# Optimization experiments

Measured on AMD Instinct MI355X. Metric: run time of the kernel, lower is better.

## Reference

```python
import jax, jax.numpy as jnp
import numpy as np

B, NX, NY = 4, 128, 128
DIM, DH, HEADS, LATENT, DOUT = 128, 64, 8, 64, 128
KM = 3
KD = DH * KM          # per-head low-rank-kernel dim (192)
SCALING = 1.0         # kernel_multiplier<=4 and softmax=False -> scaling_factor
ROT_SCALE = 64.0      # 1/min_freq of continuous RotaryEmbedding (min_freq=1/64)
EPS = 1e-5


def layer_norm(x, g, b):
    m = x.mean(-1, keepdims=True)
    v = jnp.var(x, axis=-1, keepdims=True)
    return (x - m) * jax.lax.rsqrt(v + EPS) * g + b


def pooling_reducer(x, Win, g, b, W1, b1, W2, b2):
    # x: [b, n, m, c] -> mean over axis 2 -> PreNorm(MLP with gated GELU) -> [b, n, latent]
    h = (x @ Win).mean(axis=2)
    h = layer_norm(h, g, b)
    h = h @ W1 + b1
    c = h.shape[-1] // 2
    h = jax.nn.gelu(h[..., :c], approximate=False) * h[..., c:]
    return h @ W2 + b2


def rotary(t, pos):
    # t: [b,h,n,d], pos: [n] continuous coordinates
    d = t.shape[-1]
    inv_freq = 1.0 / (10000.0 ** (jnp.arange(0, d, 2, dtype=jnp.float32) / d))
    f = (pos * ROT_SCALE)[:, None] * inv_freq          # [n, d//2]
    f = jnp.concatenate([f, f], axis=-1)               # [n, d]
    cos, sin = jnp.cos(f), jnp.sin(f)
    x1, x2 = jnp.split(t, 2, axis=-1)
    rot = jnp.concatenate([-x2, x1], axis=-1)          # rotate_half (half-split variant)
    return t * cos + rot * sin


def low_rank_kernel(u, pos, Wqk):
    # u: [b, n, latent] -> kernel K: [b, h, n, n]
    b, n, _ = u.shape
    qk = u @ Wqk                                       # [b, n, 2*h*KD]
    q, k = jnp.split(qk, 2, axis=-1)
    q = q.reshape(b, n, HEADS, KD).transpose(0, 2, 1, 3)
    k = k.reshape(b, n, HEADS, KD).transpose(0, 2, 1, 3)
    q = rotary(q, pos)
    k = rotary(k, pos)
    return jnp.einsum('bhid,bhjd->bhij', q, k) * SCALING


def setup_inputs():
    key = jax.random.key(0)
    ks = jax.random.split(key, 16)
    s = 0.02
    def rn(k, shape):
        return jax.random.normal(k, shape, dtype=jnp.float32) * s
    return {
        'u': jax.random.normal(ks[0], (B, NX, NY, DIM), dtype=jnp.float32),
        'pos_x': jnp.sort(jax.random.uniform(ks[1], (NX,), dtype=jnp.float32)),
        'pos_y': jnp.sort(jax.random.uniform(ks[2], (NY,), dtype=jnp.float32)),
        'ln_g': jnp.ones((DIM,), jnp.float32),
        'ln_b': jnp.zeros((DIM,), jnp.float32),
        'Wv': rn(ks[3], (DIM, HEADS * DH)),
        'Win': rn(ks[4], (DIM, DIM)),
        'px_Win': rn(ks[5], (DIM, DIM)),
        'px_g': jnp.ones((DIM,), jnp.float32),
        'px_b': jnp.zeros((DIM,), jnp.float32),
        'px_W1': rn(ks[6], (DIM, 2 * DIM)),
        'px_b1': jnp.zeros((2 * DIM,), jnp.float32),
        'px_W2': rn(ks[7], (DIM, LATENT)),
        'px_b2': jnp.zeros((LATENT,), jnp.float32),
        'py_Win': rn(ks[8], (DIM, DIM)),
        'py_g': jnp.ones((DIM,), jnp.float32),
        'py_b': jnp.zeros((DIM,), jnp.float32),
        'py_W1': rn(ks[9], (DIM, 2 * DIM)),
        'py_b1': jnp.zeros((2 * DIM,), jnp.float32),
        'py_W2': rn(ks[10], (DIM, LATENT)),
        'py_b2': jnp.zeros((LATENT,), jnp.float32),
        'Wqk_x': rn(ks[11], (LATENT, 2 * HEADS * KD)),
        'Wqk_y': rn(ks[12], (LATENT, 2 * HEADS * KD)),
        'Wo1': rn(ks[13], (HEADS * DH, DOUT)),
        'Wo2': rn(ks[14], (DOUT, DOUT)),
    }


def reference(u, pos_x, pos_y, ln_g, ln_b, Wv, Win,
              px_Win, px_g, px_b, px_W1, px_b1, px_W2, px_b2,
              py_Win, py_g, py_b, py_W1, py_b1, py_W2, py_b2,
              Wqk_x, Wqk_y, Wo1, Wo2):
    un = layer_norm(u, ln_g, ln_b)                      # [b,nx,ny,dim]
    v = un @ Wv                                         # [b,nx,ny,h*dh]
    ui = un @ Win
    ux = pooling_reducer(ui, px_Win, px_g, px_b, px_W1, px_b1, px_W2, px_b2)                       # [b,nx,L]
    uy = pooling_reducer(ui.transpose(0, 2, 1, 3), py_Win, py_g, py_b, py_W1, py_b1, py_W2, py_b2)  # [b,ny,L]
    kx = low_rank_kernel(ux, pos_x, Wqk_x)              # [b,h,nx,nx]
    ky = low_rank_kernel(uy, pos_y, Wqk_y)              # [b,h,ny,ny]
    b, nx, ny, _ = u.shape
    vphi = v.reshape(b, nx, ny, HEADS, DH).transpose(0, 3, 1, 2, 4)   # b h i l c
    t = jnp.einsum('bhij,bhjmc->bhimc', kx, vphi)       # attend along x axis
    t = jnp.einsum('bhlm,bhimc->bhilc', ky, t)          # attend along y axis
    t = t.transpose(0, 2, 3, 1, 4).reshape(b, nx, ny, HEADS * DH)
    # InstanceNorm2d applied to a channels-LAST tensor (as in the original repo):
    # torch treats dim1 (nx) as channels, normalizing over (ny, h*dh) per (b, nx), no affine.
    m = t.mean(axis=(2, 3), keepdims=True)
    var = t.var(axis=(2, 3), keepdims=True)
    t = (t - m) * jax.lax.rsqrt(var + EPS)
    h = jax.nn.gelu(t @ Wo1, approximate=False)
    return h @ Wo2
```

## Files before the change

kernel.cpp:

```cpp
#include <hip/hip_runtime.h>
#include <math.h>

#define ROWS 65536
#define KDD 192

typedef __attribute__((ext_vector_type(8))) short bfrag;
typedef __attribute__((ext_vector_type(4))) float facc;

__device__ inline unsigned short bf16r(float x) {
  union { float f; unsigned u; } v; v.f = x;
  unsigned r = v.u + 0x7fffu + ((v.u >> 16) & 1u);
  return (unsigned short)(r >> 16);
}
__device__ inline float bf2f(unsigned short h) {
  union { unsigned u; float f; } v; v.u = ((unsigned)h) << 16; return v.f;
}
__device__ inline float gelu_f(float x) {
  return x * 0.5f * (1.f + erff(x * 0.70710678f));
}

__global__ __launch_bounds__(128) void k_ln(const float* __restrict__ x,
                                            const float* __restrict__ g,
                                            const float* __restrict__ bb,
                                            unsigned short* __restrict__ y) {
  int row = blockIdx.x;
  int t = threadIdx.x;
  float v = x[(size_t)row * 128 + t];
  float s = v, s2 = v * v;
  for (int off = 32; off > 0; off >>= 1) {
    s += __shfl_down(s, off, 64);
    s2 += __shfl_down(s2, off, 64);
  }
  __shared__ float ps[2], ps2[2];
  int wid = t >> 6, lane = t & 63;
  if (lane == 0) { ps[wid] = s; ps2[wid] = s2; }
  __syncthreads();
  float S = ps[0] + ps[1], S2 = ps2[0] + ps2[1];
  float mean = S * (1.f / 128.f);
  float var = S2 * (1.f / 128.f) - mean * mean;
  float r = rsqrtf(var + 1e-5f);
  y[(size_t)row * 128 + t] = bf16r((v - mean) * r * g[t] + bb[t]);
}

__global__ __launch_bounds__(128) void k_means(const unsigned short* __restrict__ un,
                                               float* __restrict__ mx, float* __restrict__ my) {
  int blk = blockIdx.x;
  int c = threadIdx.x;
  if (blk < 512) {
    const unsigned short* p = un + (size_t)blk * 16384 + c;
    float s = 0;
    for (int j = 0; j < 128; j++) s += bf2f(p[(size_t)j * 128]);
    mx[(size_t)blk * 128 + c] = s * (1.f / 128.f);
  } else {
    int bj = blk - 512;
    int b = bj >> 7, j = bj & 127;
    const unsigned short* p = un + (size_t)b * 2097152 + (size_t)j * 128 + c;
    float s = 0;
    for (int i = 0; i < 128; i++) s += bf2f(p[(size_t)i * 16384]);
    my[(size_t)bj * 128 + c] = s * (1.f / 128.f);
  }
}

__global__ __launch_bounds__(256) void k_wprep(const float* __restrict__ Wv,
                                               const float* __restrict__ Wo1,
                                               const float* __restrict__ Wo2,
                                               unsigned short* __restrict__ WvT,
                                               unsigned short* __restrict__ Wo1T,
                                               unsigned short* __restrict__ Wo2T,
                                               float* __restrict__ scol) {
  int blk = blockIdx.x, t = threadIdx.x;
  if (blk < 256) {
    int idx = blk * 256 + t;
    int c = idx >> 7, r = idx & 127;
    WvT[(size_t)c * 128 + r] = bf16r(Wv[(size_t)r * 512 + c]);
  } else if (blk < 512) {
    int idx = (blk - 256) * 256 + t;
    int n = idx >> 9, k = idx & 511;
    Wo1T[(size_t)n * 512 + k] = bf16r(Wo1[(size_t)k * 128 + n]);
  } else if (blk < 576) {
    int idx = (blk - 512) * 256 + t;
    int n = idx >> 7, k = idx & 127;
    Wo2T[n * 128 + k] = bf16r(Wo2[k * 128 + n]);
  } else {
    if (t < 128) {
      float a = 0;
      for (int k = 0; k < 512; k++) a += bf2f(bf16r(Wo1[k * 128 + t]));
      scol[t] = a;
    }
  }
}

__global__ __launch_bounds__(256) void k_gemmz(const float* __restrict__ A0,
                                               const float* __restrict__ B0,
                                               float* __restrict__ C0,
                                               const float* __restrict__ A1,
                                               const float* __restrict__ B1,
                                               float* __restrict__ C1,
                                               int K, int lda, int ldb, int ldc) {
  const float* A = blockIdx.z ? A1 : A0;
  const float* Bm = blockIdx.z ? B1 : B0;
  float* C = blockIdx.z ? C1 : C0;
  __shared__ float As[16][64];
  __shared__ float Bs[16][64];
  int tid = threadIdx.x;
  int n0 = blockIdx.x * 64, m0 = blockIdx.y * 64;
  int tx = tid & 15, ty = tid >> 4;
  float acc[4][4] = {};
  int la_m = tid >> 2, la_k = (tid & 3) * 4;
  int lb_k = tid >> 4, lb_n = (tid & 15) * 4;
  for (int k0 = 0; k0 < K; k0 += 16) {
    float4 a4 = *(const float4*)(A + (size_t)(m0 + la_m) * lda + k0 + la_k);
    As[la_k + 0][la_m] = a4.x; As[la_k + 1][la_m] = a4.y;
    As[la_k + 2][la_m] = a4.z; As[la_k + 3][la_m] = a4.w;
    float4 b4 = *(const float4*)(Bm + (size_t)(k0 + lb_k) * ldb + n0 + lb_n);
    *(float4*)&Bs[lb_k][lb_n] = b4;
    __syncthreads();
#pragma unroll
    for (int kk = 0; kk < 16; kk++) {
      float4 av = *(const float4*)&As[kk][ty * 4];
      float4 bv = *(const float4*)&Bs[kk][tx * 4];
      float a[4] = {av.x, av.y, av.z, av.w};
      float b[4] = {bv.x, bv.y, bv.z, bv.w};
#pragma unroll
      for (int i = 0; i < 4; i++)
#pragma unroll
        for (int j = 0; j < 4; j++) acc[i][j] += a[i] * b[j];
    }
    __syncthreads();
  }
#pragma unroll
  for (int i = 0; i < 4; i++) {
    float4 o;
    o.x = acc[i][0]; o.y = acc[i][1]; o.z = acc[i][2]; o.w = acc[i][3];
    *(float4*)(C + (size_t)(m0 + ty * 4 + i) * ldc + n0 + tx * 4) = o;
  }
}

__global__ __launch_bounds__(128) void k_pool2(const float* __restrict__ in0, const float* __restrict__ in1,
                                               const float* __restrict__ Wc0, const float* __restrict__ Wc1,
                                               const float* __restrict__ g0, const float* __restrict__ g1,
                                               const float* __restrict__ bb0, const float* __restrict__ bb1,
                                               const float* __restrict__ W10, const float* __restrict__ W11,
                                               const float* __restrict__ b10, const float* __restrict__ b11,
                                               const float* __restrict__ W20, const float* __restrict__ W21,
                                               const float* __restrict__ b20, const float* __restrict__ b21,
                                               float* __restrict__ o0, float* __restrict__ o1) {
  int sel = blockIdx.y;
  const float* in = sel ? in1 : in0;  const float* Wc = sel ? Wc1 : Wc0;
  const float* g = sel ? g1 : g0;     const float* bb = sel ? bb1 : bb0;
  const float* W1 = sel ? W11 : W10;  const float* b1 = sel ? b11 : b10;
  const float* W2 = sel ? W21 : W20;  const float* b2 = sel ? b21 : b20;
  float* out = sel ? o1 : o0;
  int row = blockIdx.x;
  int t = threadIdx.x;
  __shared__ float xin[128], h1[128], h3[128];
  __shared__ float ps[2], ps2[2];
  xin[t] = in[(size_t)row * 128 + t];
  __syncthreads();
  float a = 0;
  for (int k = 0; k < 128; k++) a += xin[k] * Wc[k * 128 + t];
  float s = a, s2 = a * a;
  for (int off = 32; off > 0; off >>= 1) {
    s += __shfl_down(s, off, 64);
    s2 += __shfl_down(s2, off, 64);
  }
  if ((t & 63) == 0) { ps[t >> 6] = s; ps2[t >> 6] = s2; }
  __syncthreads();
  float S = ps[0] + ps[1], S2 = ps2[0] + ps2[1];
  float mean = S * (1.f / 128.f);
  float var = S2 * (1.f / 128.f) - mean * mean;
  float r = rsqrtf(var + 1e-5f);
  h1[t] = (a - mean) * r * g[t] + bb[t];
  __syncthreads();
  float u1 = b1[t], u2 = b1[t + 128];
  for (int k = 0; k < 128; k++) {
    float hv = h1[k];
    u1 += hv * W1[k * 256 + t];
    u2 += hv * W1[k * 256 + t + 128];
  }
  h3[t] = gelu_f(u1) * u2;
  __syncthreads();
  if (t < 64) {
    float o = b2[t];
    for (int k = 0; k < 128; k++) o += h3[k] * W2[k * 64 + t];
    out[(size_t)row * 64 + t] = o;
  }
}

__global__ __launch_bounds__(192) void k_rot2(const float* __restrict__ qk0, const float* __restrict__ qk1,
                                              const float* __restrict__ pos0, const float* __restrict__ pos1,
                                              float* __restrict__ qr0, float* __restrict__ qr1,
                                              float* __restrict__ kr0, float* __restrict__ kr1) {
  int sel = blockIdx.y;
  const float* qk = sel ? qk1 : qk0;
  const float* pos = sel ? pos1 : pos0;
  float* qr = sel ? qr1 : qr0;
  float* kr = sel ? kr1 : kr0;
  int bn = blockIdx.x;
  int b = bn >> 7, n = bn & 127;
  int d = threadIdx.x;
  int fi = d % 96;
  float inv = expf(-logf(10000.f) * ((float)fi / 96.f));
  float f = pos[n] * 64.f * inv;
  float cs = cosf(f), sn = sinf(f);
  int partner = d < 96 ? d + 96 : d - 96;
  float sgn = d < 96 ? -1.f : 1.f;
  for (int h = 0; h < 8; h++) {
    float q = qk[(size_t)bn * 3072 + h * 192 + d];
    float qp = qk[(size_t)bn * 3072 + h * 192 + partner];
    float kx = qk[(size_t)bn * 3072 + 1536 + h * 192 + d];
    float kp = qk[(size_t)bn * 3072 + 1536 + h * 192 + partner];
    size_t o = ((size_t)(b * 8 + h) * 128 + n) * 192 + d;
    qr[o] = q * cs + sgn * qp * sn;
    kr[o] = kx * cs + sgn * kp * sn;
  }
}

__global__ __launch_bounds__(256) void k_qkt2(const float* __restrict__ Q0, const float* __restrict__ K0,
                                              unsigned short* __restrict__ C0,
                                              const float* __restrict__ Q1, const float* __restrict__ K1,
                                              unsigned short* __restrict__ C1) {
  int z = blockIdx.z;
  int bh = z & 31;
  const float* Qb = (z < 32 ? Q0 : Q1) + (size_t)bh * 128 * KDD;
  const float* Kb = (z < 32 ? K0 : K1) + (size_t)bh * 128 * KDD;
  unsigned short* Cb = (z < 32 ? C0 : C1) + (size_t)bh * 128 * 128;
  __shared__ float As[16][64];
  __shared__ float Bs[16][64];
  int tid = threadIdx.x;
  int i0 = blockIdx.y * 64, j0 = blockIdx.x * 64;
  int tx = tid & 15, ty = tid >> 4;
  float acc[4][4] = {};
  int l_m = tid >> 2, l_k = (tid & 3) * 4;
  for (int k0 = 0; k0 < KDD; k0 += 16) {
    float4 a4 = *(const float4*)(Qb + (size_t)(i0 + l_m) * KDD + k0 + l_k);
    As[l_k + 0][l_m] = a4.x; As[l_k + 1][l_m] = a4.y;
    As[l_k + 2][l_m] = a4.z; As[l_k + 3][l_m] = a4.w;
    float4 b4 = *(const float4*)(Kb + (size_t)(j0 + l_m) * KDD + k0 + l_k);
    Bs[l_k + 0][l_m] = b4.x; Bs[l_k + 1][l_m] = b4.y;
    Bs[l_k + 2][l_m] = b4.z; Bs[l_k + 3][l_m] = b4.w;
    __syncthreads();
#pragma unroll
    for (int kk = 0; kk < 16; kk++) {
      float4 av = *(const float4*)&As[kk][ty * 4];
      float4 bv = *(const float4*)&Bs[kk][tx * 4];
      float a[4] = {av.x, av.y, av.z, av.w};
      float b[4] = {bv.x, bv.y, bv.z, bv.w};
#pragma unroll
      for (int i = 0; i < 4; i++)
#pragma unroll
        for (int j = 0; j < 4; j++) acc[i][j] += a[i] * b[j];
    }
    __syncthreads();
  }
#pragma unroll
  for (int i = 0; i < 4; i++) {
    unsigned h0 = bf16r(acc[i][0]), h1 = bf16r(acc[i][1]);
    unsigned h2 = bf16r(acc[i][2]), h3 = bf16r(acc[i][3]);
    uint2 pk;
    pk.x = h0 | (h1 << 16);
    pk.y = h2 | (h3 << 16);
    *(uint2*)(Cb + (size_t)(i0 + ty * 4 + i) * 128 + j0 + tx * 4) = pk;
  }
}


__global__ __launch_bounds__(256) void k_vt(const unsigned short* __restrict__ WvT,
                                            const unsigned short* __restrict__ un,
                                            unsigned short* __restrict__ vT) {
  int nt = blockIdx.x;
  int mt = blockIdx.y;
  __shared__ __align__(16) unsigned short As[16384];
  __shared__ __align__(16) unsigned short Bs[16384];
  int tid = threadIdx.x;
  int w = tid >> 6, lane = tid & 63, quad = lane >> 4, l16 = lane & 15;
  {
    int r = tid >> 1, half = tid & 1;
    const unsigned short* sa = WvT + (size_t)(mt * 128 + r) * 128 + half * 64;
    const unsigned short* sbp = un + (size_t)(nt * 128 + r) * 128 + half * 64;
#pragma unroll
    for (int q = 0; q < 8; q++) {
      int c8 = half * 8 + q;
      int ph = ((c8 ^ (r & 15)) << 3);
      *(uint4*)&As[r * 128 + ph] = *(const uint4*)(sa + q * 8);
      *(uint4*)&Bs[r * 128 + ph] = *(const uint4*)(sbp + q * 8);
    }
  }
  __syncthreads();
  facc zf = {0.f, 0.f, 0.f, 0.f};
  facc acc[2][8];
#pragma unroll
  for (int a = 0; a < 2; a++)
#pragma unroll
    for (int bq = 0; bq < 8; bq++) acc[a][bq] = zf;
#pragma unroll
  for (int k0 = 0; k0 < 4; k0++) {
    bfrag av[2];
#pragma unroll
    for (int it = 0; it < 2; it++) {
      int row = (w + it * 4) * 16 + l16;
      av[it] = *(const bfrag*)&As[row * 128 + ((((k0 * 4 + quad) ^ l16)) << 3)];
    }
#pragma unroll
    for (int nt8 = 0; nt8 < 8; nt8++) {
      int row = nt8 * 16 + l16;
      bfrag bv = *(const bfrag*)&Bs[row * 128 + ((((k0 * 4 + quad) ^ l16)) << 3)];
      acc[0][nt8] = __builtin_amdgcn_mfma_f32_16x16x32_bf16(av[0], bv, acc[0][nt8], 0, 0, 0);
      acc[1][nt8] = __builtin_amdgcn_mfma_f32_16x16x32_bf16(av[1], bv, acc[1][nt8], 0, 0, 0);
    }
  }
  __syncthreads();
#pragma unroll
  for (int it = 0; it < 2; it++)
#pragma unroll
    for (int nt8 = 0; nt8 < 8; nt8++)
#pragma unroll
      for (int rr = 0; rr < 4; rr++) {
        int row = (w + it * 4) * 16 + quad * 4 + rr;
        int col = nt8 * 16 + l16;
        As[row * 128 + ((((col >> 3) ^ (row & 15)) << 3)) + (col & 7)] = bf16r(acc[it][nt8][rr]);
      }
  __syncthreads();
  {
    int r = tid >> 1, half = tid & 1;
    unsigned short* dst = vT + (size_t)(mt * 128 + r) * 65536 + (size_t)nt * 128 + half * 64;
#pragma unroll
    for (int q = 0; q < 8; q++) {
      int c8 = half * 8 + q;
      *(uint4*)(dst + q * 8) = *(const uint4*)&As[r * 128 + ((c8 ^ (r & 15)) << 3)];
    }
  }
}

__global__ __launch_bounds__(256) void k_fuse12(const unsigned short* __restrict__ kxall,
                                                const unsigned short* __restrict__ kyall,
                                                const unsigned short* __restrict__ vT,
                                                unsigned short* __restrict__ ttp,
                                                float* __restrict__ sb,
                                                float* __restrict__ s2b) {
  int blk = blockIdx.x;
  int bh = blk >> 4, strip = blk & 15;
  int b = bh >> 3, h = bh & 7;
  __shared__ __align__(16) unsigned short Ky[16384];
  __shared__ __align__(16) unsigned short Vs[16384];
  __shared__ float sL[128], s2L[128];
  int tid = threadIdx.x;
  int w = tid >> 6, lane = tid & 63, quad = lane >> 4, l16 = lane & 15;
  if (tid < 128) { sL[tid] = 0.f; s2L[tid] = 0.f; }
  {
    int r = tid >> 1, half = tid & 1;
    const unsigned short* s = kyall + (size_t)bh * 16384 + (size_t)r * 128 + half * 64;
#pragma unroll
    for (int q = 0; q < 8; q++) {
      int c8 = half * 8 + q;
      *(uint4*)&Ky[r * 128 + ((c8 ^ (r & 15)) << 3)] = *(const uint4*)(s + q * 8);
    }
  }
  uint4 axf[2][4];
#pragma unroll
  for (int it = 0; it < 2; it++) {
    int i = (w + it * 4) * 16 + l16;
#pragma unroll
    for (int k0 = 0; k0 < 4; k0++)
      axf[it][k0] = *(const uint4*)(kxall + (size_t)bh * 16384 + (size_t)i * 128 + k0 * 32 + quad * 8);
  }
  __syncthreads();
  facc zf = {0.f, 0.f, 0.f, 0.f};
  for (int cc = 0; cc < 4; cc++) {
    int c = strip * 4 + cc;
    if (cc) __syncthreads();
    {
      int r = tid >> 1, half = tid & 1;
      const unsigned short* s = vT + (size_t)(h * 64 + c) * 65536 + (size_t)b * 16384 +
                                (size_t)r * 128 + half * 64;
#pragma unroll
      for (int q = 0; q < 8; q++) {
        int c8 = half * 8 + q;
        *(uint4*)&Vs[r * 128 + ((c8 ^ (r & 15)) << 3)] = *(const uint4*)(s + q * 8);
      }
    }
    __syncthreads();
    facc a1[2][8];
#pragma unroll
    for (int a = 0; a < 2; a++)
#pragma unroll
      for (int bq = 0; bq < 8; bq++) a1[a][bq] = zf;
#pragma unroll
    for (int k0 = 0; k0 < 4; k0++) {
      bfrag av[2];
#pragma unroll
      for (int it = 0; it < 2; it++) {
        int row = (w + it * 4) * 16 + l16;
        av[it] = *(const bfrag*)&Vs[row * 128 + (((k0 * 4 + quad) ^ l16) << 3)];
      }
#pragma unroll
      for (int lt = 0; lt < 8; lt++) {
        int row = lt * 16 + l16;
        bfrag bv = *(const bfrag*)&Ky[row * 128 + (((k0 * 4 + quad) ^ l16) << 3)];
        a1[0][lt] = __builtin_amdgcn_mfma_f32_16x16x32_bf16(av[0], bv, a1[0][lt], 0, 0, 0);
        a1[1][lt] = __builtin_amdgcn_mfma_f32_16x16x32_bf16(av[1], bv, a1[1][lt], 0, 0, 0);
      }
    }
    __syncthreads();
#pragma unroll
    for (int it = 0; it < 2; it++)
#pragma unroll
      for (int lt = 0; lt < 8; lt++)
#pragma unroll
        for (int rr = 0; rr < 4; rr++) {
          int j = (w + it * 4) * 16 + quad * 4 + rr;
          int l = lt * 16 + l16;
          Vs[l * 128 + (((j >> 3) ^ (l & 15)) << 3) + (j & 7)] = bf16r(a1[it][lt][rr]);
        }
    __syncthreads();
    facc a2[2][8];
#pragma unroll
    for (int a = 0; a < 2; a++)
#pragma unroll
      for (int bq = 0; bq < 8; bq++) a2[a][bq] = zf;
#pragma unroll
    for (int k0 = 0; k0 < 4; k0++) {
      bfrag av0 = *(const bfrag*)&axf[0][k0];
      bfrag av1 = *(const bfrag*)&axf[1][k0];
#pragma unroll
      for (int lt = 0; lt < 8; lt++) {
        int row = lt * 16 + l16;
        bfrag bv = *(const bfrag*)&Vs[row * 128 + (((k0 * 4 + quad) ^ l16) << 3)];
        a2[0][lt] = __builtin_amdgcn_mfma_f32_16x16x32_bf16(av0, bv, a2[0][lt], 0, 0, 0);
        a2[1][lt] = __builtin_amdgcn_mfma_f32_16x16x32_bf16(av1, bv, a2[1][lt], 0, 0, 0);
      }
    }
    __syncthreads();
#pragma unroll
    for (int it = 0; it < 2; it++)
#pragma unroll
      for (int lt = 0; lt < 8; lt++)
#pragma unroll
        for (int rr = 0; rr < 4; rr++) {
          int i = (w + it * 4) * 16 + quad * 4 + rr;
          int l = lt * 16 + l16;
          Vs[i * 128 + (((l >> 3) ^ (i & 15)) << 3) + (l & 7)] = bf16r(a2[it][lt][rr]);
        }
    __syncthreads();
    {
      int r = tid >> 1, half = tid & 1;
      float s = 0.f, s2 = 0.f;
      unsigned short* dst = ttp + ((size_t)(bh * 64 + c) * 128 + r) * 128 + half * 64;
#pragma unroll
      for (int q = 0; q < 8; q++) {
        int c8 = half * 8 + q;
        uint4 v = *(const uint4*)&Vs[r * 128 + ((c8 ^ (r & 15)) << 3)];
        *(uint4*)(dst + q * 8) = v;
        unsigned short* pv = (unsigned short*)&v;
#pragma unroll
        for (int e = 0; e < 8; e++) { float f = bf2f(pv[e]); s += f; s2 += f * f; }
      }
      atomicAdd(&sL[r], s);
      atomicAdd(&s2L[r], s2);
    }
  }
  __syncthreads();
  if (tid < 128) {
    atomicAdd(&sb[b * 128 + tid], sL[tid]);
    atomicAdd(&s2b[b * 128 + tid], s2L[tid]);
  }
}

__global__ __launch_bounds__(256) void k_tail2(const unsigned short* __restrict__ ttp,
                                               const unsigned short* __restrict__ Wo1T,
                                               const unsigned short* __restrict__ Wo2T,
                                               float* __restrict__ out,
                                               const float* __restrict__ sb,
                                               const float* __restrict__ s2b,
                                               const float* __restrict__ sc) {
  int blk = blockIdx.x;
  int b = blk >> 7, i = blk & 127;
  __shared__ __align__(16) unsigned short As[16384];
  __shared__ __align__(16) unsigned short Bs[16384];
  int tid = threadIdx.x;
  int w = tid >> 6, lane = tid & 63, quad = lane >> 4, l16 = lane & 15;
  facc zf = {0.f, 0.f, 0.f, 0.f};
  facc a1[2][8];
#pragma unroll
  for (int a = 0; a < 2; a++)
#pragma unroll
    for (int bq = 0; bq < 8; bq++) a1[a][bq] = zf;
  for (int kc = 0; kc < 4; kc++) {
    if (kc) __syncthreads();
    {
      int r = tid >> 1, half = tid & 1;
      int hc = kc * 128 + r;
      const unsigned short* src = ttp + (((size_t)(b * 8 + (hc >> 6)) * 64 + (hc & 63)) * 128 + i) * 128 + half * 64;
#pragma unroll
      for (int q = 0; q < 8; q++) {
        uint4 v = *(const uint4*)(src + q * 8);
        unsigned short* pv = (unsigned short*)&v;
#pragma unroll
        for (int e = 0; e < 8; e++) {
          int l = half * 64 + q * 8 + e;
          As[l * 128 + (((r >> 3) ^ (l & 15)) << 3) + (r & 7)] = pv[e];
        }
      }
      const unsigned short* sB = Wo1T + (size_t)r * 512 + kc * 128 + half * 64;
#pragma unroll
      for (int q = 0; q < 8; q++) {
        int c8 = half * 8 + q;
        *(uint4*)&Bs[r * 128 + ((c8 ^ (r & 15)) << 3)] = *(const uint4*)(sB + q * 8);
      }
    }
    __syncthreads();
#pragma unroll
    for (int k0 = 0; k0 < 4; k0++) {
      bfrag av[2];
#pragma unroll
      for (int it = 0; it < 2; it++) {
        int row = (w + it * 4) * 16 + l16;
        av[it] = *(const bfrag*)&As[row * 128 + (((k0 * 4 + quad) ^ l16) << 3)];
      }
#pragma unroll
      for (int nt = 0; nt < 8; nt++) {
        int row = nt * 16 + l16;
        bfrag bv = *(const bfrag*)&Bs[row * 128 + (((k0 * 4 + quad) ^ l16) << 3)];
        a1[0][nt] = __builtin_amdgcn_mfma_f32_16x16x32_bf16(av[0], bv, a1[0][nt], 0, 0, 0);
        a1[1][nt] = __builtin_amdgcn_mfma_f32_16x16x32_bf16(av[1], bv, a1[1][nt], 0, 0, 0);
      }
    }
  }
  float S = sb[b * 128 + i], S2 = s2b[b * 128 + i];
  float mean = S * (1.f / 65536.f);
  float var = S2 * (1.f / 65536.f) - mean * mean;
  float rs = rsqrtf(var + 1e-5f);
  __syncthreads();
#pragma unroll
  for (int it = 0; it < 2; it++)
#pragma unroll
    for (int nt = 0; nt < 8; nt++) {
      int n1 = nt * 16 + l16;
      float scn = sc[n1];
#pragma unroll
      for (int rr = 0; rr < 4; rr++) {
        int l = (w + it * 4) * 16 + quad * 4 + rr;
        float val = (a1[it][nt][rr] - mean * scn) * rs;
        As[l * 128 + (((n1 >> 3) ^ (l & 15)) << 3) + (n1 & 7)] = bf16r(gelu_f(val));
      }
    }
  {
    int r = tid >> 1, half = tid & 1;
    const unsigned short* sB = Wo2T + (size_t)r * 128 + half * 64;
#pragma unroll
    for (int q = 0; q < 8; q++) {
      int c8 = half * 8 + q;
      *(uint4*)&Bs[r * 128 + ((c8 ^ (r & 15)) << 3)] = *(const uint4*)(sB + q * 8);
    }
  }
  __syncthreads();
  facc a2[2][8];
#pragma unroll
  for (int a = 0; a < 2; a++)
#pragma unroll
    for (int bq = 0; bq < 8; bq++) a2[a][bq] = zf;
#pragma unroll
  for (int k0 = 0; k0 < 4; k0++) {
    bfrag av[2];
#pragma unroll
    for (int it = 0; it < 2; it++) {
      int row = (w + it * 4) * 16 + l16;
      av[it] = *(const bfrag*)&As[row * 128 + (((k0 * 4 + quad) ^ l16) << 3)];
    }
#pragma unroll
    for (int nt = 0; nt < 8; nt++) {
      int row = nt * 16 + l16;
      bfrag bv = *(const bfrag*)&Bs[row * 128 + (((k0 * 4 + quad) ^ l16) << 3)];
      a2[0][nt] = __builtin_amdgcn_mfma_f32_16x16x32_bf16(av[0], bv, a2[0][nt], 0, 0, 0);
      a2[1][nt] = __builtin_amdgcn_mfma_f32_16x16x32_bf16(av[1], bv, a2[1][nt], 0, 0, 0);
    }
  }
#pragma unroll
  for (int it = 0; it < 2; it++)
#pragma unroll
    for (int nt = 0; nt < 8; nt++) {
      int n2 = nt * 16 + l16;
#pragma unroll
      for (int rr = 0; rr < 4; rr++) {
        int l = (w + it * 4) * 16 + quad * 4 + rr;
        out[((size_t)(b * 16384 + i * 128 + l)) * 128 + n2] = a2[it][nt][rr];
      }
    }
}

extern "C" void kernel_launch(void* const* d_in, const int* in_sizes, int n_in,
                              void* d_out, int out_size, void* d_ws, size_t ws_size,
                              hipStream_t stream) {
  const float* u = (const float*)d_in[0];
  const float* pos_x = (const float*)d_in[1];
  const float* pos_y = (const float*)d_in[2];
  const float* ln_g = (const float*)d_in[3];
  const float* ln_b = (const float*)d_in[4];
  const float* Wv = (const float*)d_in[5];
  const float* Win = (const float*)d_in[6];
  const float* px_Win = (const float*)d_in[7];
  const float* px_g = (const float*)d_in[8];
  const float* px_b = (const float*)d_in[9];
  const float* px_W1 = (const float*)d_in[10];
  const float* px_b1 = (const float*)d_in[11];
  const float* px_W2 = (const float*)d_in[12];
  const float* px_b2 = (const float*)d_in[13];
  const float* py_Win = (const float*)d_in[14];
  const float* py_g = (const float*)d_in[15];
  const float* py_b = (const float*)d_in[16];
  const float* py_W1 = (const float*)d_in[17];
  const float* py_b1 = (const float*)d_in[18];
  const float* py_W2 = (const float*)d_in[19];
  const float* py_b2 = (const float*)d_in[20];
  const float* Wqk_x = (const float*)d_in[21];
  const float* Wqk_y = (const float*)d_in[22];
  const float* Wo1 = (const float*)d_in[23];
  const float* Wo2 = (const float*)d_in[24];
  float* out = (float*)d_out;

  const size_t NEED = 44868736;
  if (ws_size < NEED * sizeof(float)) return;
  float* ws = (float*)d_ws;
  unsigned short* un_bf = (unsigned short*)ws;
  unsigned short* vT    = (unsigned short*)(ws + 4194304);
  unsigned short* ttp   = (unsigned short*)(ws + 20971520);
  float* small = ws + 37748736;
  float* mun_x = small;
  float* mun_y = small + 65536;
  float* Wcx   = small + 131072;
  float* Wcy   = small + 147456;
  float* ux    = small + 163840;
  float* uy    = small + 196608;
  float* qkx   = small + 229376;
  float* qky   = small + 1802240;
  float* qrx   = small + 3375104;
  float* krx   = small + 4161536;
  float* qry   = small + 4947968;
  float* kry   = small + 5734400;
  unsigned short* kx_bf = (unsigned short*)(small + 6520832);
  unsigned short* ky_bf = (unsigned short*)(small + 6782976);
  unsigned short* WvT   = (unsigned short*)(small + 7045120);
  unsigned short* Wo1T  = (unsigned short*)(small + 7077888);
  unsigned short* Wo2T  = (unsigned short*)(small + 7110656);
  float* sbuf  = small + 7118848;
  float* s2buf = small + 7119360;
  float* scol  = small + 7119872;

  hipMemsetAsync(sbuf, 0, 1024 * sizeof(float), stream);

  k_ln<<<ROWS, 128, 0, stream>>>(u, ln_g, ln_b, un_bf);
  k_means<<<1024, 128, 0, stream>>>(un_bf, mun_x, mun_y);
  k_wprep<<<577, 256, 0, stream>>>(Wv, Wo1, Wo2, WvT, Wo1T, Wo2T, scol);
  k_gemmz<<<dim3(2, 2, 2), 256, 0, stream>>>(Win, px_Win, Wcx, Win, py_Win, Wcy,
                                             128, 128, 128, 128);
  k_pool2<<<dim3(512, 2), 128, 0, stream>>>(mun_x, mun_y, Wcx, Wcy, px_g, py_g, px_b, py_b,
                                            px_W1, py_W1, px_b1, py_b1, px_W2, py_W2,
                                            px_b2, py_b2, ux, uy);
  k_gemmz<<<dim3(48, 8, 2), 256, 0, stream>>>(ux, Wqk_x, qkx, uy, Wqk_y, qky,
                                              64, 64, 3072, 3072);
  k_rot2<<<dim3(512, 2), 192, 0, stream>>>(qkx, qky, pos_x, pos_y, qrx, qry, krx, kry);
  k_qkt2<<<dim3(2, 2, 64), 256, 0, stream>>>(qrx, krx, kx_bf, qry, kry, ky_bf);

  k_vt<<<dim3(512, 4), 256, 0, stream>>>(WvT, un_bf, vT);
  k_fuse12<<<512, 256, 0, stream>>>(kx_bf, ky_bf, vT, ttp, sbuf, s2buf);
  k_tail2<<<512, 256, 0, stream>>>(ttp, Wo1T, Wo2T, out, sbuf, s2buf, scol);
}
```

Before: 350.1 us.

## Restructure fused axial-attention kernel with 2x2 warp tiling and direct-to-LDS loads

After: 337.2 us. -3.7%, faster.

```diff
diff --git a/kernel.cpp b/kernel.cpp
--- a/kernel.cpp
+++ b/kernel.cpp
@@ -17,6 +17,11 @@
 }
 __device__ inline float gelu_f(float x) {
   return x * 0.5f * (1.f + erff(x * 0.70710678f));
+}
+__device__ __forceinline__ void gload16(const void* g, void* l) {
+  __builtin_amdgcn_global_load_lds((const __attribute__((address_space(1))) unsigned int*)g,
+                                   (__attribute__((address_space(3))) unsigned int*)l,
+                                   16, 0, 0);
 }
 
 __global__ __launch_bounds__(128) void k_ln(const float* __restrict__ x,
@@ -332,137 +337,148 @@
   }
 }
 
-__global__ __launch_bounds__(256) void k_fuse12(const unsigned short* __restrict__ kxall,
-                                                const unsigned short* __restrict__ kyall,
-                                                const unsigned short* __restrict__ vT,
-                                                unsigned short* __restrict__ ttp,
-                                                float* __restrict__ sb,
-                                                float* __restrict__ s2b) {
+__global__ __launch_bounds__(256, 2) void k_fuse12(const unsigned short* __restrict__ kxall,
+                                                   const unsigned short* __restrict__ kyall,
+                                                   const unsigned short* __restrict__ vT,
+                                                   unsigned short* __restrict__ ttp,
+                                                   float* __restrict__ sb,
+                                                   float* __restrict__ s2b) {
   int blk = blockIdx.x;
   int bh = blk >> 4, strip = blk & 15;
   int b = bh >> 3, h = bh & 7;
   __shared__ __align__(16) unsigned short Ky[16384];
   __shared__ __align__(16) unsigned short Vs[16384];
-  __shared__ float sL[128], s2L[128];
   int tid = threadIdx.x;
   int w = tid >> 6, lane = tid & 63, quad = lane >> 4, l16 = lane & 15;
-  if (tid < 128) { sL[tid] = 0.f; s2L[tid] = 0.f; }
+  int wr = w >> 1, wc = w & 1;
+
   {
-    int r = tid >> 1, half = tid & 1;
-    const unsigned short* s = kyall + (size_t)bh * 16384 + (size_t)r * 128 + half * 64;
+    const unsigned short* kb = kyall + (size_t)bh * 16384;
 #pragma unroll
     for (int q = 0; q < 8; q++) {
-      int c8 = half * 8 + q;
-      *(uint4*)&Ky[r * 128 + ((c8 ^ (r & 15)) << 3)] = *(const uint4*)(s + q * 8);
-    }
-  }
-  uint4 axf[2][4];
-#pragma unroll
-  for (int it = 0; it < 2; it++) {
-    int i = (w + it * 4) * 16 + l16;
-#pragma unroll
-    for (int k0 = 0; k0 < 4; k0++)
-      axf[it][k0] = *(const uint4*)(kxall + (size_t)bh * 16384 + (size_t)i * 128 + k0 * 32 + quad * 8);
-  }
-  __syncthreads();
+      int rbase = w * 32 + q * 4;
+      int r = rbase + quad;
+      gload16(kb + (size_t)r * 128 + ((l16 ^ (r & 15)) << 3), &Ky[rbase * 128]);
+    }
+  }
+  bfrag axf[4][4];
+  {
+    const unsigned short* xb = kxall + (size_t)bh * 16384;
+#pragma unroll
+    for (int it = 0; it < 4; it++) {
+      int i = (wr * 4 + it) * 16 + l16;
+#pragma unroll
+      for (int k0 = 0; k0 < 4; k0++)
+        axf[it][k0] = *(const bfrag*)(xb + (size_t)i * 128 + k0 * 32 + quad * 8);
+    }
+  }
+
+  float s[4] = {0.f, 0.f, 0.f, 0.f}, s2[4] = {0.f, 0.f, 0.f, 0.f};
   facc zf = {0.f, 0.f, 0.f, 0.f};
+
   for (int cc = 0; cc < 4; cc++) {
     int c = strip * 4 + cc;
     if (cc) __syncthreads();
     {
-      int r = tid >> 1, half = tid & 1;
-      const unsigned short* s = vT + (size_t)(h * 64 + c) * 65536 + (size_t)b * 16384 +
-                                (size_t)r * 128 + half * 64;
+      const unsigned short* vb = vT + (size_t)(h * 64 + c) * 65536 + (size_t)b * 16384;
 #pragma unroll
       for (int q = 0; q < 8; q++) {
-        int c8 = half * 8 + q;
-        *(uint4*)&Vs[r * 128 + ((c8 ^ (r & 15)) << 3)] = *(const uint4*)(s + q * 8);
-      }
-    }
-    __syncthreads();
-    facc a1[2][8];
-#pragma unroll
-    for (int a = 0; a < 2; a++)
-#pragma unroll
-      for (int bq = 0; bq < 8; bq++) a1[a][bq] = zf;
+        int rbase = w * 32 + q * 4;
+        int r = rbase + quad;
+        gload16(vb + (size_t)r * 128 + ((l16 ^ (r & 15)) << 3), &Vs[rbase * 128]);
+      }
+    }
+    __syncthreads();
+
+    facc a1[4][4];
+#pragma unroll
+    for (int xt = 0; xt < 4; xt++)
+#pragma unroll
+      for (int lt = 0; lt < 4; lt++) a1[xt][lt] = zf;
 #pragma unroll
     for (int k0 = 0; k0 < 4; k0++) {
-      bfrag av[2];
-#pragma unroll
-      for (int it = 0; it < 2; it++) {
-        int row = (w + it * 4) * 16 + l16;
-        av[it] = *(const bfrag*)&Vs[row * 128 + (((k0 * 4 + quad) ^ l16) << 3)];
-      }
-#pragma unroll
-      for (int lt = 0; lt < 8; lt++) {
-        int row = lt * 16 + l16;
-        bfrag bv = *(const bfrag*)&Ky[row * 128 + (((k0 * 4 + quad) ^ l16) << 3)];
-        a1[0][lt] = __builtin_amdgcn_mfma_f32_16x16x32_bf16(av[0], bv, a1[0][lt], 0, 0, 0);
-        a1[1][lt] = __builtin_amdgcn_mfma_f32_16x16x32_bf16(av[1], bv, a1[1][lt], 0, 0, 0);
-      }
-    }
-    __syncthreads();
-#pragma unroll
-    for (int it = 0; it < 2; it++)
-#pragma unroll
-      for (int lt = 0; lt < 8; lt++)
-#pragma unroll
-        for (int rr = 0; rr < 4; rr++) {
-          int j = (w + it * 4) * 16 + quad * 4 + rr;
-          int l = lt * 16 + l16;
-          Vs[l * 128 + (((j >> 3) ^ (l & 15)) << 3) + (j & 7)] = bf16r(a1[it][lt][rr]);
+      int chunk = ((k0 * 4 + quad) ^ l16) << 3;
+      bfrag av[4], bv[4];
+#pragma unroll
+      for (int xt = 0; xt < 4; xt++)
+        av[xt] = *(const bfrag*)&Vs[((wr * 4 + xt) * 16 + l16) * 128 + chunk];
+#pragma unroll
+      for (int lt = 0; lt < 4; lt++)
+        bv[lt] = *(const bfrag*)&Ky[((wc * 4 + lt) * 16 + l16) * 128 + chunk];
+      __builtin_amdgcn_s_setprio(1);
+#pragma unroll
+      for (int xt = 0; xt < 4; xt++)
+#pragma unroll
+        for (int lt = 0; lt < 4; lt++)
+          a1[xt][lt] = __builtin_amdgcn_mfma_f32_16x16x32_bf16(av[xt], bv[lt], a1[xt][lt], 0, 0, 0);
+      __builtin_amdgcn_s_setprio(0);
+    }
+    __syncthreads();
+#pragma unroll
+    for (int xt = 0; xt < 4; xt++) {
+      int xc = (wr * 4 + xt) * 2 + (quad >> 1);
+      int xo = (quad & 1) * 4;
+#pragma unroll
+      for (int lt = 0; lt < 4; lt++) {
+        int l = (wc * 4 + lt) * 16 + l16;
+        unsigned p0 = (unsigned)bf16r(a1[xt][lt][0]) | ((unsigned)bf16r(a1[xt][lt][1]) << 16);
+        unsigned p1 = (unsigned)bf16r(a1[xt][lt][2]) | ((unsigned)bf16r(a1[xt][lt][3]) << 16);
+        uint2 p; p.x = p0; p.y = p1;
+        *(uint2*)&Vs[l * 128 + ((xc ^ (l & 15)) << 3) + xo] = p;
+      }
+    }
+    __syncthreads();
+
+    facc a2[4][4];
+#pragma unroll
+    for (int st = 0; st < 4; st++)
+#pragma unroll
+      for (int it = 0; it < 4; it++) a2[st][it] = zf;
+#pragma unroll
+    for (int k0 = 0; k0 < 4; k0++) {
+      int chunk = ((k0 * 4 + quad) ^ l16) << 3;
+      bfrag sv[4];
+#pragma unroll
+      for (int st = 0; st < 4; st++)
+        sv[st] = *(const bfrag*)&Vs[((wc * 4 + st) * 16 + l16) * 128 + chunk];
+      __builtin_amdgcn_s_setprio(1);
+#pragma unroll
+      for (int st = 0; st < 4; st++)
+#pragma unroll
+        for (int it = 0; it < 4; it++)
+          a2[st][it] = __builtin_amdgcn_mfma_f32_16x16x32_bf16(sv[st], axf[it][k0], a2[st][it], 0, 0, 0);
+      __builtin_amdgcn_s_setprio(0);
+    }
+    {
+      unsigned short* dst = ttp + ((size_t)(bh * 64 + c) << 14);
+#pragma unroll
+      for (int st = 0; st < 4; st++) {
+        int l0 = (wc * 4 + st) * 16 + quad * 4;
+#pragma unroll
+        for (int it = 0; it < 4; it++) {
+          int i = (wr * 4 + it) * 16 + l16;
+          float f0 = a2[st][it][0], f1 = a2[st][it][1];
+          float f2 = a2[st][it][2], f3 = a2[st][it][3];
+          unsigned p0 = (unsigned)bf16r(f0) | ((unsigned)bf16r(f1) << 16);
+          unsigned p1 = (unsigned)bf16r(f2) | ((unsigned)bf16r(f3) << 16);
+          uint2 p; p.x = p0; p.y = p1;
+          *(uint2*)(dst + (size_t)i * 128 + l0) = p;
+          s[it] += (f0 + f1) + (f2 + f3);
+          s2[it] += f0 * f0 + f1 * f1 + f2 * f2 + f3 * f3;
         }
-    __syncthreads();
-    facc a2[2][8];
-#pragma unroll
-    for (int a = 0; a < 2; a++)
-#pragma unroll
-      for (int bq = 0; bq < 8; bq++) a2[a][bq] = zf;
-#pragma unroll
-    for (int k0 = 0; k0 < 4; k0++) {
-      bfrag av0 = *(const bfrag*)&axf[0][k0];
-      bfrag av1 = *(const bfrag*)&axf[1][k0];
-#pragma unroll
-      for (int lt = 0; lt < 8; lt++) {
-        int row = lt * 16 + l16;
-        bfrag bv = *(const bfrag*)&Vs[row * 128 + (((k0 * 4 + quad) ^ l16) << 3)];
-        a2[0][lt] = __builtin_amdgcn_mfma_f32_16x16x32_bf16(av0, bv, a2[0][lt], 0, 0, 0);
-        a2[1][lt] = __builtin_amdgcn_mfma_f32_16x16x32_bf16(av1, bv, a2[1][lt], 0, 0, 0);
-      }
-    }
-    __syncthreads();
-#pragma unroll
-    for (int it = 0; it < 2; it++)
-#pragma unroll
-      for (int lt = 0; lt < 8; lt++)
-#pragma unroll
-        for (int rr = 0; rr < 4; rr++) {
-          int i = (w + it * 4) * 16 + quad * 4 + rr;
-          int l = lt * 16 + l16;
-          Vs[i * 128 + (((l >> 3) ^ (i & 15)) << 3) + (l & 7)] = bf16r(a2[it][lt][rr]);
-        }
-    __syncthreads();
-    {
-      int r = tid >> 1, half = tid & 1;
-      float s = 0.f, s2 = 0.f;
-      unsigned short* dst = ttp + ((size_t)(bh * 64 + c) * 128 + r) * 128 + half * 64;
-#pragma unroll
-      for (int q = 0; q < 8; q++) {
-        int c8 = half * 8 + q;
-        uint4 v = *(const uint4*)&Vs[r * 128 + ((c8 ^ (r & 15)) << 3)];
-        *(uint4*)(dst + q * 8) = v;
-        unsigned short* pv = (unsigned short*)&v;
-#pragma unroll
-        for (int e = 0; e < 8; e++) { float f = bf2f(pv[e]); s += f; s2 += f * f; }
-      }
-      atomicAdd(&sL[r], s);
-      atomicAdd(&s2L[r], s2);
-    }
-  }
-  __syncthreads();
-  if (tid < 128) {
-    atomicAdd(&sb[b * 128 + tid], sL[tid]);
-    atomicAdd(&s2b[b * 128 + tid], s2L[tid]);
+      }
+    }
+  }
+#pragma unroll
+  for (int it = 0; it < 4; it++) {
+    float v = s[it], v2 = s2[it];
+    v += __shfl_xor(v, 16, 64);  v += __shfl_xor(v, 32, 64);
+    v2 += __shfl_xor(v2, 16, 64); v2 += __shfl_xor(v2, 32, 64);
+    if (quad == 0) {
+      int i = (wr * 4 + it) * 16 + l16;
+      atomicAdd(&sb[b * 128 + i], v);
+      atomicAdd(&s2b[b * 128 + i], v2);
+    }
   }
 }
 
```
